# Kernel optimization log

Measured on AMD Instinct MI355X. Metric: run time of the kernel, lower is better.

## Reference

```python
import jax, jax.numpy as jnp
import numpy as np

B, L, I, O = 32, 512, 1024, 1024
TMIN, TMAX = -8.0, -2.0


def setup_inputs() -> dict:
    key = jax.random.key(0)
    k1, k2, k3, k4, k5 = jax.random.split(key, 5)
    x = jax.random.normal(k1, (B, L, I), dtype=jnp.float32)
    weight_mean = jax.random.normal(k2, (O, I), dtype=jnp.float32) * 0.02
    # matches torch init: -rand * (tmax - tmin) + tmin
    weight_logvar = -jax.random.uniform(k3, (O, I), dtype=jnp.float32) * (TMAX - TMIN) + TMIN
    bias = jax.random.normal(k4, (O,), dtype=jnp.float32) * 0.02
    # standard-normal reparameterization noise (the torch module's randn)
    noise = jax.random.normal(k5, (B, O, I), dtype=jnp.float32)
    return {"x": x, "weight_mean": weight_mean, "weight_logvar": weight_logvar,
            "bias": bias, "noise": noise}


def reference(x, weight_mean, weight_logvar, bias, noise):
    # per-sample sampled weights: W_b = mean + eps_b * sqrt(exp(logvar))
    w = weight_mean + noise * jnp.exp(0.5 * weight_logvar)  # (B, O, I)
    # bmm(x, W^T) + bias  ->  (B, L, O)
    return jnp.einsum('bli,boi->blo', x, w) + bias
```

## Files before the change

### kernel.cpp

```cpp
#include <hip/hip_runtime.h>
#include <hip/hip_bf16.h>
#include <stdint.h>

#define B_ 32
#define L_ 512
#define I_ 1024
#define O_ 1024
#define NKT 16

typedef float  f32x4  __attribute__((ext_vector_type(4)));
typedef __bf16 bf16x4 __attribute__((ext_vector_type(4)));
typedef __bf16 bf16x8 __attribute__((ext_vector_type(8)));

#define CFENCE() asm volatile("" ::: "memory")
#define BARRIER() do { CFENCE(); __builtin_amdgcn_s_barrier(); CFENCE(); } while (0)

__device__ __forceinline__ void gload_lds16(const void* g, void* l) {
    __builtin_amdgcn_global_load_lds(
        (const __attribute__((address_space(1))) uint32_t*)(uintptr_t)g,
        (__attribute__((address_space(3))) uint32_t*)(uint32_t)(uintptr_t)l,
        16, 0, 0);
}

__global__ void gen_w_kernel(const float* __restrict__ wmean,
                             const float* __restrict__ wlv,
                             const float* __restrict__ noise,
                             __bf16* __restrict__ W)
{
    const int n4 = B_ * O_ * I_ / 4;
    const int stride = gridDim.x * blockDim.x;
    for (int i = blockIdx.x * blockDim.x + threadIdx.x; i < n4; i += stride) {
        const int mi = i & (O_ * I_ / 4 - 1);
        const f32x4 m4 = *(const f32x4*)(wmean + (size_t)mi * 4);
        const f32x4 l4 = *(const f32x4*)(wlv   + (size_t)mi * 4);
        const f32x4 e4 = *(const f32x4*)(noise + (size_t)i  * 4);
        bf16x4 w;
        w[0] = (__bf16)(m4[0] + e4[0] * __expf(0.5f * l4[0]));
        w[1] = (__bf16)(m4[1] + e4[1] * __expf(0.5f * l4[1]));
        w[2] = (__bf16)(m4[2] + e4[2] * __expf(0.5f * l4[2]));
        w[3] = (__bf16)(m4[3] + e4[3] * __expf(0.5f * l4[3]));
        *(bf16x4*)(W + (size_t)i * 4) = w;
    }
}

__global__ void cvt_x_kernel(const float* __restrict__ x, __bf16* __restrict__ xb)
{
    const int n4 = B_ * L_ * I_ / 4;
    const int stride = gridDim.x * blockDim.x;
    for (int i = blockIdx.x * blockDim.x + threadIdx.x; i < n4; i += stride) {
        const f32x4 v = *(const f32x4*)(x + (size_t)i * 4);
        bf16x4 w;
        w[0] = (__bf16)v[0]; w[1] = (__bf16)v[1];
        w[2] = (__bf16)v[2]; w[3] = (__bf16)v[3];
        *(bf16x4*)(xb + (size_t)i * 4) = w;
    }
}

__global__ __launch_bounds__(512, 2) void gemm_8ph(const __bf16* __restrict__ xb,
                                                   const __bf16* __restrict__ W,
                                                   const float* __restrict__ bias,
                                                   float* __restrict__ out)
{
    __shared__ __align__(16) char smem[131072];

    const int bid = ((int)blockIdx.x & 7) * 32 + ((int)blockIdx.x >> 3);
    const int b   = bid >> 3;
    const int mt  = (bid >> 2) & 1;
    const int nt  = bid & 3;

    const int tid  = threadIdx.x;
    const int wid  = tid >> 6, lane = tid & 63;
    const int wr   = wid >> 2;
    const int wc   = wid & 3;
    const int hr   = lane & 15;
    const int kq   = lane >> 4;

    const int P0c = tid, P1c = tid + 512;
    const int r0 = P0c >> 3, c0 = (P0c & 7) ^ (r0 & 7);
    const int r1 = P1c >> 3, c1 = (P1c & 7) ^ (r1 & 7);
    const size_t gO0 = (size_t)r0 * I_ + c0 * 8;
    const size_t gO1 = (size_t)r1 * I_ + c1 * 8;

    const __bf16* ax = xb + (size_t)b * L_ * I_ + (size_t)(mt * 256) * I_;
    const __bf16* bw = W  + (size_t)b * O_ * I_ + (size_t)(nt * 256) * I_;

#define STG(srcp, slotbyte) do {                                          \
        gload_lds16((srcp) + gO0, smem + (slotbyte) + tid * 16);          \
        gload_lds16((srcp) + gO1, smem + (slotbyte) + 8192 + tid * 16);   \
    } while (0)

    const int pc0 = (0 + kq) ^ (hr & 7);
    const int pc1 = (4 + kq) ^ (hr & 7);
    const int aob = wr * 16384 + hr * 128;
    const int bob = (wc >> 1) * 16384 + (wc & 1) * 8192 + hr * 128;

    f32x4 acc[8][4];
    #pragma unroll
    for (int m = 0; m < 8; ++m)
        #pragma unroll
        for (int n = 0; n < 4; ++n)
            acc[m][n] = (f32x4)(0.0f);

#define LDA(mb, dA_) do {                                                             \
        _Pragma("unroll")                                                             \
        for (int mm = 0; mm < 2; ++mm) {                                              \
            af[mm][0] = *(const bf16x8*)(smem + (dA_) + aob + ((mb)+mm)*2048 + pc0*16); \
            af[mm][1] = *(const bf16x8*)(smem + (dA_) + aob + ((mb)+mm)*2048 + pc1*16); \
        } } while (0)

#define DO_MFMA(mb) do {                                                              \
        __builtin_amdgcn_s_setprio(1);                                                \
        _Pragma("unroll")                                                             \
        for (int mm = 0; mm < 2; ++mm)                                                \
            _Pragma("unroll")                                                         \
            for (int n = 0; n < 4; ++n)                                               \
                _Pragma("unroll")                                                     \
                for (int kk = 0; kk < 2; ++kk)                                        \
                    acc[(mb)+mm][n] = __builtin_amdgcn_mfma_f32_16x16x32_bf16(        \
                        af[mm][kk], bfr[n][kk], acc[(mb)+mm][n], 0, 0, 0);            \
        __builtin_amdgcn_s_setprio(0); } while (0)

    STG(bw,                         65536 + 0);
    STG(bw + (size_t)128 * I_,      65536 + 16384);
    STG(ax,                         0);
    STG(ax + (size_t)128 * I_,      16384);
    STG(bw + 64,                    65536 + 32768);
    STG(bw + (size_t)128 * I_ + 64, 65536 + 32768 + 16384);
    CFENCE(); asm volatile("s_waitcnt vmcnt(4)" ::: "memory");
    BARRIER();

    for (int t = 0; t < NKT; ++t) {
        const int d  = t & 1;
        const int dA = d * 32768;
        const int dB = 65536 + d * 32768;
        const int dN = (d ^ 1) * 32768;
        bf16x8 af[2][2], bfr[4][2];

        #pragma unroll
        for (int n = 0; n < 4; ++n) {
            bfr[n][0] = *(const bf16x8*)(smem + dB + bob + n * 2048 + pc0 * 16);
            bfr[n][1] = *(const bf16x8*)(smem + dB + bob + n * 2048 + pc1 * 16);
        }
        LDA(0, dA);
        if (t + 1 < NKT) STG(ax + (size_t)(t + 1) * 64, dN);
        BARRIER();
        DO_MFMA(0);
        BARRIER();

        LDA(2, dA);
        if (t + 1 < NKT) STG(ax + (size_t)128 * I_ + (size_t)(t + 1) * 64, dN + 16384);
        BARRIER();
        DO_MFMA(2);
        BARRIER();

        LDA(4, dA);
        if (t + 2 < NKT) STG(bw + (size_t)(t + 2) * 64, dB);
        BARRIER();
        DO_MFMA(4);
        BARRIER();

        LDA(6, dA);
        if (t + 2 < NKT) STG(bw + (size_t)128 * I_ + (size_t)(t + 2) * 64, dB + 16384);
        if (t < NKT - 2)       { CFENCE(); asm volatile("s_waitcnt vmcnt(4)" ::: "memory"); }
        else if (t == NKT - 2) { CFENCE(); asm volatile("s_waitcnt vmcnt(0)" ::: "memory"); }
        BARRIER();
        DO_MFMA(6);
        BARRIER();
    }
#undef STG
#undef LDA
#undef DO_MFMA

    {
        float* eb = (float*)smem;
        const f32x4 bias4 = *(const f32x4*)(bias + nt * 256 + lane * 4);
        float* ob = out + ((size_t)b * L_ + (size_t)(mt * 256)) * O_ + nt * 256;
        #pragma unroll
        for (int r = 0; r < 4; ++r) {
            BARRIER();
            if (wr == (r >> 1)) {
                #pragma unroll
                for (int mm = 0; mm < 4; ++mm)
                    #pragma unroll
                    for (int n = 0; n < 4; ++n) {
                        const int col = wc * 64 + n * 16 + hr;
                        #pragma unroll
                        for (int j = 0; j < 4; ++j)
                            eb[(mm * 16 + kq * 4 + j) * 260 + col] = acc[(r & 1) * 4 + mm][n][j];
                    }
            }
            BARRIER();
            #pragma unroll
            for (int rr = 0; rr < 8; ++rr) {
                const int row = wid * 8 + rr;
                f32x4 v = *(const f32x4*)&eb[row * 260 + lane * 4];
                v += bias4;
                *(f32x4*)&ob[(size_t)(r * 64 + row) * O_ + lane * 4] = v;
            }
        }
    }
}

#define LDSPAD 40
__global__ void bayes_gemm_fused(const float* __restrict__ x,
                                 const float* __restrict__ wmean,
                                 const float* __restrict__ wlogvar,
                                 const float* __restrict__ bias,
                                 const float* __restrict__ noise,
                                 float* __restrict__ out)
{
    __shared__ __bf16 As[128 * LDSPAD];
    __shared__ __bf16 Bs[128 * LDSPAD];
    const int bid  = blockIdx.x;
    const int b    = bid >> 5;
    const int mt   = (bid >> 3) & 3;
    const int nt   = bid & 7;
    const int t    = threadIdx.x;
    const int wave = t >> 6, lane = t & 63;
    const int wr   = wave >> 1, wc = wave & 1;
    const int hr   = lane & 15, kq = lane >> 4;
    const float* xb = x     + (size_t)b * L_ * I_;
    const float* nb = noise + (size_t)b * O_ * I_;
    f32x4 acc[4][4];
    #pragma unroll
    for (int m = 0; m < 4; ++m)
        #pragma unroll
        for (int n = 0; n < 4; ++n) acc[m][n] = (f32x4)(0.0f);
    for (int k0 = 0; k0 < I_; k0 += 32) {
        #pragma unroll
        for (int j = 0; j < 4; ++j) {
            const int s = t + j * 256, row = s >> 3, q = s & 7;
            const float4 v = *(const float4*)(xb + (size_t)(mt * 128 + row) * I_ + k0 + q * 4);
            __bf16* dst = &As[row * LDSPAD + q * 4];
            dst[0] = (__bf16)v.x; dst[1] = (__bf16)v.y; dst[2] = (__bf16)v.z; dst[3] = (__bf16)v.w;
        }
        #pragma unroll
        for (int j = 0; j < 4; ++j) {
            const int s = t + j * 256, row = s >> 3, q = s & 7;
            const size_t off = (size_t)(nt * 128 + row) * I_ + k0 + q * 4;
            const float4 m4 = *(const float4*)(wmean + off);
            const float4 l4 = *(const float4*)(wlogvar + off);
            const float4 n4 = *(const float4*)(nb + off);
            __bf16* dst = &Bs[row * LDSPAD + q * 4];
            dst[0] = (__bf16)(m4.x + n4.x * __expf(0.5f * l4.x));
            dst[1] = (__bf16)(m4.y + n4.y * __expf(0.5f * l4.y));
            dst[2] = (__bf16)(m4.z + n4.z * __expf(0.5f * l4.z));
            dst[3] = (__bf16)(m4.w + n4.w * __expf(0.5f * l4.w));
        }
        __syncthreads();
        bf16x8 af[4], bfr[4];
        #pragma unroll
        for (int m = 0; m < 4; ++m)
            af[m] = *(const bf16x8*)&As[(wr * 64 + m * 16 + hr) * LDSPAD + kq * 8];
        #pragma unroll
        for (int n = 0; n < 4; ++n)
            bfr[n] = *(const bf16x8*)&Bs[(wc * 64 + n * 16 + hr) * LDSPAD + kq * 8];
        #pragma unroll
        for (int m = 0; m < 4; ++m)
            #pragma unroll
            for (int n = 0; n < 4; ++n)
                acc[m][n] = __builtin_amdgcn_mfma_f32_16x16x32_bf16(af[m], bfr[n], acc[m][n], 0, 0, 0);
        __syncthreads();
    }
    float* ob = out + (size_t)b * L_ * O_;
    #pragma unroll
    for (int n = 0; n < 4; ++n) {
        const int col = nt * 128 + wc * 64 + n * 16 + hr;
        const float bv = bias[col];
        #pragma unroll
        for (int m = 0; m < 4; ++m) {
            const int row0 = mt * 128 + wr * 64 + m * 16 + kq * 4;
            #pragma unroll
            for (int j = 0; j < 4; ++j)
                ob[(size_t)(row0 + j) * O_ + col] = acc[m][n][j] + bv;
        }
    }
}

extern "C" void kernel_launch(void* const* d_in, const int* in_sizes, int n_in,
                              void* d_out, int out_size, void* d_ws, size_t ws_size,
                              hipStream_t stream) {
    const float* x       = (const float*)d_in[0];
    const float* wmean   = (const float*)d_in[1];
    const float* wlogvar = (const float*)d_in[2];
    const float* bias    = (const float*)d_in[3];
    const float* noise   = (const float*)d_in[4];
    float* out           = (float*)d_out;

    const size_t w_bytes  = (size_t)B_ * O_ * I_ * 2;
    const size_t xb_bytes = (size_t)B_ * L_ * I_ * 2;

    if (ws_size >= w_bytes + xb_bytes) {
        __bf16* W    = (__bf16*)d_ws;
        __bf16* xbuf = (__bf16*)((char*)d_ws + w_bytes);
        gen_w_kernel<<<dim3(2048), dim3(256), 0, stream>>>(wmean, wlogvar, noise, W);
        cvt_x_kernel<<<dim3(1024), dim3(256), 0, stream>>>(x, xbuf);
        gemm_8ph<<<dim3(256), dim3(512), 0, stream>>>(xbuf, W, bias, out);
    } else {
        bayes_gemm_fused<<<dim3(1024), dim3(256), 0, stream>>>(
            x, wmean, wlogvar, bias, noise, out);
    }
}
```

Measured before the change: 107.7 us.

## Fuse weight sampling and x conversion into GEMM staging loop

Drops the separate kernels that materialised full per-batch bf16 sampled weights and bf16 x in workspace. The GEMM now loads fp32 x and noise plus precomputed bf16 mean and sigma tables, forms W and converts x in registers, and writes them to LDS. This removes the round trip of the large intermediate tensors through HBM. In exchange it drops async global-to-LDS loads, adds register pressure and VALU work inside the main loop, and rounds mean and sigma to bf16 before combining them.

```diff
diff --git a/kernel.cpp b/kernel.cpp
--- a/kernel.cpp
+++ b/kernel.cpp
@@ -14,52 +14,30 @@
 
 #define CFENCE() asm volatile("" ::: "memory")
 #define BARRIER() do { CFENCE(); __builtin_amdgcn_s_barrier(); CFENCE(); } while (0)
-
-__device__ __forceinline__ void gload_lds16(const void* g, void* l) {
-    __builtin_amdgcn_global_load_lds(
-        (const __attribute__((address_space(1))) uint32_t*)(uintptr_t)g,
-        (__attribute__((address_space(3))) uint32_t*)(uint32_t)(uintptr_t)l,
-        16, 0, 0);
+#define LGKM0()  asm volatile("s_waitcnt lgkmcnt(0)" ::: "memory")
+
+__global__ void gen_ms_kernel(const float* __restrict__ wmean, const float* __restrict__ wlv,
+                              __bf16* __restrict__ mz, __bf16* __restrict__ sg)
+{
+    const int i = blockIdx.x * blockDim.x + threadIdx.x;
+    const f32x4 m = *(const f32x4*)(wmean + (size_t)i * 4);
+    const f32x4 l = *(const f32x4*)(wlv   + (size_t)i * 4);
+    bf16x4 mb, sb;
+    #pragma unroll
+    for (int e = 0; e < 4; ++e) {
+        mb[e] = (__bf16)m[e];
+        sb[e] = (__bf16)__expf(0.5f * l[e]);
+    }
+    *(bf16x4*)(mz + (size_t)i * 4) = mb;
+    *(bf16x4*)(sg + (size_t)i * 4) = sb;
 }
 
-__global__ void gen_w_kernel(const float* __restrict__ wmean,
-                             const float* __restrict__ wlv,
-                             const float* __restrict__ noise,
-                             __bf16* __restrict__ W)
-{
-    const int n4 = B_ * O_ * I_ / 4;
-    const int stride = gridDim.x * blockDim.x;
-    for (int i = blockIdx.x * blockDim.x + threadIdx.x; i < n4; i += stride) {
-        const int mi = i & (O_ * I_ / 4 - 1);
-        const f32x4 m4 = *(const f32x4*)(wmean + (size_t)mi * 4);
-        const f32x4 l4 = *(const f32x4*)(wlv   + (size_t)mi * 4);
-        const f32x4 e4 = *(const f32x4*)(noise + (size_t)i  * 4);
-        bf16x4 w;
-        w[0] = (__bf16)(m4[0] + e4[0] * __expf(0.5f * l4[0]));
-        w[1] = (__bf16)(m4[1] + e4[1] * __expf(0.5f * l4[1]));
-        w[2] = (__bf16)(m4[2] + e4[2] * __expf(0.5f * l4[2]));
-        w[3] = (__bf16)(m4[3] + e4[3] * __expf(0.5f * l4[3]));
-        *(bf16x4*)(W + (size_t)i * 4) = w;
-    }
-}
-
-__global__ void cvt_x_kernel(const float* __restrict__ x, __bf16* __restrict__ xb)
-{
-    const int n4 = B_ * L_ * I_ / 4;
-    const int stride = gridDim.x * blockDim.x;
-    for (int i = blockIdx.x * blockDim.x + threadIdx.x; i < n4; i += stride) {
-        const f32x4 v = *(const f32x4*)(x + (size_t)i * 4);
-        bf16x4 w;
-        w[0] = (__bf16)v[0]; w[1] = (__bf16)v[1];
-        w[2] = (__bf16)v[2]; w[3] = (__bf16)v[3];
-        *(bf16x4*)(xb + (size_t)i * 4) = w;
-    }
-}
-
-__global__ __launch_bounds__(512, 2) void gemm_8ph(const __bf16* __restrict__ xb,
-                                                   const __bf16* __restrict__ W,
-                                                   const float* __restrict__ bias,
-                                                   float* __restrict__ out)
+__global__ __launch_bounds__(512, 2) void fused_gemm(const float* __restrict__ x,
+                                                     const float* __restrict__ noise,
+                                                     const __bf16* __restrict__ mz,
+                                                     const __bf16* __restrict__ sg,
+                                                     const float* __restrict__ bias,
+                                                     float* __restrict__ out)
 {
     __shared__ __align__(16) char smem[131072];
 
@@ -75,18 +53,69 @@
     const int hr   = lane & 15;
     const int kq   = lane >> 4;
 
-    const int P0c = tid, P1c = tid + 512;
-    const int r0 = P0c >> 3, c0 = (P0c & 7) ^ (r0 & 7);
-    const int r1 = P1c >> 3, c1 = (P1c & 7) ^ (r1 & 7);
-    const size_t gO0 = (size_t)r0 * I_ + c0 * 8;
-    const size_t gO1 = (size_t)r1 * I_ + c1 * 8;
-
-    const __bf16* ax = xb + (size_t)b * L_ * I_ + (size_t)(mt * 256) * I_;
-    const __bf16* bw = W  + (size_t)b * O_ * I_ + (size_t)(nt * 256) * I_;
-
-#define STG(srcp, slotbyte) do {                                          \
-        gload_lds16((srcp) + gO0, smem + (slotbyte) + tid * 16);          \
-        gload_lds16((srcp) + gO1, smem + (slotbyte) + 8192 + tid * 16);   \
+    const int r0 = tid >> 3, c0 = tid & 7;
+    const size_t gOa = (size_t)r0 * I_ + c0 * 8;
+    const size_t gOb = gOa + (size_t)64 * I_;
+    const int wba = r0 * 128 + ((c0 ^ (r0 & 7)) * 16);
+    #define HOFW ((size_t)128 * I_)
+
+    const float*  axB = x     + ((size_t)b * L_ + mt * 256) * I_;
+    const float*  nzB = noise + ((size_t)b * O_ + nt * 256) * I_;
+    const __bf16* mzB = mz    + (size_t)(nt * 256) * I_;
+    const __bf16* sgB = sg    + (size_t)(nt * 256) * I_;
+
+    bf16x8 sBm0, sBm1, sBs0, sBs1;
+    f32x4  sBn00, sBn01, sBn10, sBn11;
+    f32x4  sA00, sA01, sA02, sA03, sA10, sA11, sA12, sA13;
+
+#define B_ISSUE(hko) do {                                                  \
+        sBm0  = *(const bf16x8*)(mzB + (hko) + gOa);                       \
+        sBm1  = *(const bf16x8*)(mzB + (hko) + gOb);                       \
+        sBs0  = *(const bf16x8*)(sgB + (hko) + gOa);                       \
+        sBs1  = *(const bf16x8*)(sgB + (hko) + gOb);                       \
+        sBn00 = *(const f32x4*)(nzB + (hko) + gOa);                        \
+        sBn01 = *(const f32x4*)(nzB + (hko) + gOa + 4);                    \
+        sBn10 = *(const f32x4*)(nzB + (hko) + gOb);                        \
+        sBn11 = *(const f32x4*)(nzB + (hko) + gOb + 4);                    \
+    } while (0)
+
+#define B_WRITE(slot) do {                                                 \
+        bf16x8 w0_, w1_;                                                   \
+        _Pragma("unroll")                                                  \
+        for (int e = 0; e < 4; ++e) {                                      \
+            w0_[e]   = (__bf16)((float)sBm0[e]   + sBn00[e] * (float)sBs0[e]);   \
+            w0_[e+4] = (__bf16)((float)sBm0[e+4] + sBn01[e] * (float)sBs0[e+4]); \
+            w1_[e]   = (__bf16)((float)sBm1[e]   + sBn10[e] * (float)sBs1[e]);   \
+            w1_[e+4] = (__bf16)((float)sBm1[e+4] + sBn11[e] * (float)sBs1[e+4]); \
+        }                                                                  \
+        *(bf16x8*)(smem + (slot) + wba)        = w0_;                      \
+        *(bf16x8*)(smem + (slot) + wba + 8192) = w1_;                      \
+    } while (0)
+
+#define A_ISSUE(ko_) do {                                                  \
+        sA00 = *(const f32x4*)(axB + (ko_) + gOa);                         \
+        sA01 = *(const f32x4*)(axB + (ko_) + gOa + 4);                     \
+        sA02 = *(const f32x4*)(axB + (ko_) + gOb);                         \
+        sA03 = *(const f32x4*)(axB + (ko_) + gOb + 4);                     \
+        sA10 = *(const f32x4*)(axB + (ko_) + HOFW + gOa);                  \
+        sA11 = *(const f32x4*)(axB + (ko_) + HOFW + gOa + 4);              \
+        sA12 = *(const f32x4*)(axB + (ko_) + HOFW + gOb);                  \
+        sA13 = *(const f32x4*)(axB + (ko_) + HOFW + gOb + 4);              \
+    } while (0)
+
+#define A_WRITE(dw) do {                                                   \
+        bf16x8 a0_, a1_, a2_, a3_;                                         \
+        _Pragma("unroll")                                                  \
+        for (int e = 0; e < 4; ++e) {                                      \
+            a0_[e] = (__bf16)sA00[e]; a0_[e+4] = (__bf16)sA01[e];          \
+            a1_[e] = (__bf16)sA02[e]; a1_[e+4] = (__bf16)sA03[e];          \
+            a2_[e] = (__bf16)sA10[e]; a2_[e+4] = (__bf16)sA11[e];          \
+            a3_[e] = (__bf16)sA12[e]; a3_[e+4] = (__bf16)sA13[e];          \
+        }                                                                  \
+        *(bf16x8*)(smem + (dw) + wba)                = a0_;                \
+        *(bf16x8*)(smem + (dw) + wba + 8192)         = a1_;                \
+        *(bf16x8*)(smem + (dw) + 16384 + wba)        = a2_;                \
+        *(bf16x8*)(smem + (dw) + 16384 + wba + 8192) = a3_;                \
     } while (0)
 
     const int pc0 = (0 + kq) ^ (hr & 7);
@@ -120,20 +149,19 @@
                         af[mm][kk], bfr[n][kk], acc[(mb)+mm][n], 0, 0, 0);            \
         __builtin_amdgcn_s_setprio(0); } while (0)
 
-    STG(bw,                         65536 + 0);
-    STG(bw + (size_t)128 * I_,      65536 + 16384);
-    STG(ax,                         0);
-    STG(ax + (size_t)128 * I_,      16384);
-    STG(bw + 64,                    65536 + 32768);
-    STG(bw + (size_t)128 * I_ + 64, 65536 + 32768 + 16384);
-    CFENCE(); asm volatile("s_waitcnt vmcnt(4)" ::: "memory");
+    B_ISSUE(0);            B_WRITE(65536 + 0);
+    B_ISSUE(HOFW);         B_WRITE(65536 + 16384);
+    A_ISSUE(0);            A_WRITE(0);
+    LGKM0();
     BARRIER();
 
     for (int t = 0; t < NKT; ++t) {
-        const int d  = t & 1;
-        const int dA = d * 32768;
-        const int dB = 65536 + d * 32768;
-        const int dN = (d ^ 1) * 32768;
+        const int d   = t & 1;
+        const int dA  = d * 32768;
+        const int dB  = 65536 + d * 32768;
+        const int w32 = (d ^ 1) * 32768;
+        const bool stg = (t + 1 < NKT);
+        const size_t kon = (size_t)(t + 1) * 64;
         bf16x8 af[2][2], bfr[4][2];
 
         #pragma unroll
@@ -142,32 +170,33 @@
             bfr[n][1] = *(const bf16x8*)(smem + dB + bob + n * 2048 + pc1 * 16);
         }
         LDA(0, dA);
-        if (t + 1 < NKT) STG(ax + (size_t)(t + 1) * 64, dN);
+        if (stg) B_ISSUE(kon);
         BARRIER();
         DO_MFMA(0);
         BARRIER();
 
         LDA(2, dA);
-        if (t + 1 < NKT) STG(ax + (size_t)128 * I_ + (size_t)(t + 1) * 64, dN + 16384);
+        if (stg) { B_WRITE(65536 + w32); B_ISSUE(HOFW + kon); LGKM0(); }
         BARRIER();
         DO_MFMA(2);
         BARRIER();
 
         LDA(4, dA);
-        if (t + 2 < NKT) STG(bw + (size_t)(t + 2) * 64, dB);
+        if (stg) { A_ISSUE(kon); B_WRITE(65536 + w32 + 16384); LGKM0(); }
         BARRIER();
         DO_MFMA(4);
         BARRIER();
 
         LDA(6, dA);
-        if (t + 2 < NKT) STG(bw + (size_t)128 * I_ + (size_t)(t + 2) * 64, dB + 16384);
-        if (t < NKT - 2)       { CFENCE(); asm volatile("s_waitcnt vmcnt(4)" ::: "memory"); }
-        else if (t == NKT - 2) { CFENCE(); asm volatile("s_waitcnt vmcnt(0)" ::: "memory"); }
+        if (stg) { A_WRITE(w32); LGKM0(); }
         BARRIER();
         DO_MFMA(6);
         BARRIER();
     }
-#undef STG
+#undef B_ISSUE
+#undef B_WRITE
+#undef A_ISSUE
+#undef A_WRITE
 #undef LDA
 #undef DO_MFMA
 
@@ -287,15 +316,13 @@
     const float* noise   = (const float*)d_in[4];
     float* out           = (float*)d_out;
 
-    const size_t w_bytes  = (size_t)B_ * O_ * I_ * 2;
-    const size_t xb_bytes = (size_t)B_ * L_ * I_ * 2;
-
-    if (ws_size >= w_bytes + xb_bytes) {
-        __bf16* W    = (__bf16*)d_ws;
-        __bf16* xbuf = (__bf16*)((char*)d_ws + w_bytes);
-        gen_w_kernel<<<dim3(2048), dim3(256), 0, stream>>>(wmean, wlogvar, noise, W);
-        cvt_x_kernel<<<dim3(1024), dim3(256), 0, stream>>>(x, xbuf);
-        gemm_8ph<<<dim3(256), dim3(512), 0, stream>>>(xbuf, W, bias, out);
+    const size_t ms_bytes = (size_t)O_ * I_ * 2 * 2;
+
+    if (ws_size >= ms_bytes) {
+        __bf16* mzb = (__bf16*)d_ws;
+        __bf16* sgb = mzb + (size_t)O_ * I_;
+        gen_ms_kernel<<<dim3(O_ * I_ / 4 / 256), dim3(256), 0, stream>>>(wmean, wlogvar, mzb, sgb);
+        fused_gemm<<<dim3(256), dim3(512), 0, stream>>>(x, noise, mzb, sgb, bias, out);
     } else {
         bayes_gemm_fused<<<dim3(1024), dim3(256), 0, stream>>>(
             x, wmean, wlogvar, bias, noise, out);
```

Result: faster. 99.96 us (-7.2%).
